# Optimization experiments

Hardware: AMD Instinct MI355X
Metric: run time of the kernel (lower is better)

Reference implementation:

```python
import jax, jax.numpy as jnp
import numpy as np

B, Q, K, D = 8, 2048, 2048, 512

def setup_inputs() -> dict:
    key = jax.random.key(0)
    k1, k2, k3, k4, k5 = jax.random.split(key, 5)
    return {
        "query": jax.random.normal(k1, (B, Q, D), dtype=jnp.float32),
        "key": jax.random.normal(k2, (B, K, D), dtype=jnp.float32),
        "value": jax.random.normal(k3, (B, K, D), dtype=jnp.float32),
        "key_mask": jax.random.randint(k4, (B, K), 0, 2, dtype=jnp.int32),
        "W": jax.random.normal(k5, (D, D), dtype=jnp.float32) / np.sqrt(D),
    }

def reference(query, key, value, key_mask, W):
    # bilinear score: s[b,q,k] = query[b,q,:] @ W @ key[b,k,:]
    scale = 1.0 / jnp.sqrt(jnp.asarray(query.shape[-1], query.dtype))
    qW = jnp.einsum('bqd,de->bqe', query, W)          # [B,Q,D]
    scores = jnp.einsum('bqe,bke->bqk', qW, key)      # [B,Q,K]
    scores = jnp.where(key_mask[:, None, :] == 0, jnp.asarray(-1e20, scores.dtype), scores) * scale
    dist = jax.nn.softmax(scores, axis=-1)            # [B,Q,K]
    context = jnp.einsum('bqk,bkd->bqd', dist, value) # [B,Q,D]
    return context, dist
```

## Files before the change

### kernel.cpp

```cpp
#include <hip/hip_runtime.h>
#include <stdint.h>

#define BB 8
#define QQ 2048
#define KK 2048
#define DD 512

typedef _Float16 f16x8 __attribute__((ext_vector_type(8)));
typedef float f32x4 __attribute__((ext_vector_type(4)));

__device__ __forceinline__ unsigned short f2h(float f) {
    union { _Float16 h; unsigned short u; } x;
    x.h = (_Float16)f;
    return x.u;
}
__device__ __forceinline__ float h2f(unsigned short u) {
    union { unsigned short u; _Float16 h; } x;
    x.u = u;
    return (float)x.h;
}

__device__ __forceinline__ void async16(const unsigned short* g, unsigned short* l) {
    __builtin_amdgcn_global_load_lds(
        (const __attribute__((address_space(1))) unsigned int*)g,
        (__attribute__((address_space(3))) unsigned int*)l, 16, 0, 0);
}

__global__ __launch_bounds__(256) void cvt_f32_f16(const float* __restrict__ in,
                                                   unsigned short* __restrict__ out) {
    size_t i = ((size_t)blockIdx.x * 256 + threadIdx.x) * 8;
    float4 a = *(const float4*)(in + i);
    float4 b = *(const float4*)(in + i + 4);
    uint4 u;
    u.x = (unsigned)f2h(a.x) | ((unsigned)f2h(a.y) << 16);
    u.y = (unsigned)f2h(a.z) | ((unsigned)f2h(a.w) << 16);
    u.z = (unsigned)f2h(b.x) | ((unsigned)f2h(b.y) << 16);
    u.w = (unsigned)f2h(b.z) | ((unsigned)f2h(b.w) << 16);
    *(uint4*)(out + i) = u;
}

__global__ __launch_bounds__(256) void transpose_cvt(const float* __restrict__ in,
                                                     unsigned short* __restrict__ out,
                                                     int R, int C, long inB, long outB) {
    __shared__ float t[32][33];
    const float* ip = in + (size_t)blockIdx.z * inB;
    unsigned short* op = out + (size_t)blockIdx.z * outB;
    int x = threadIdx.x & 31, y0 = threadIdx.x >> 5;
    int c0 = blockIdx.x * 32, r0 = blockIdx.y * 32;
#pragma unroll
    for (int i = 0; i < 32; i += 8)
        t[y0 + i][x] = ip[(size_t)(r0 + y0 + i) * C + c0 + x];
    __syncthreads();
#pragma unroll
    for (int i = 0; i < 32; i += 8)
        op[(size_t)(c0 + y0 + i) * R + r0 + x] = f2h(t[x][y0 + i]);
}

template <int OUTM>
__global__ __launch_bounds__(256) void gemm_bt(const unsigned short* __restrict__ Aall,
                                               const unsigned short* __restrict__ Ball,
                                               void* __restrict__ Call,
                                               const int* __restrict__ maskAll,
                                               float* __restrict__ sums,
                                               int Kred, int lda, int ldb, int ldc,
                                               long aStride, long bStride, long cStride,
                                               int maskStride, float scale) {
    const int gx = gridDim.x, gy = gridDim.y;
    const int nwg = gx * gy * (int)gridDim.z;
    const int p = ((int)blockIdx.z * gy + (int)blockIdx.y) * gx + (int)blockIdx.x;
    const int qch = nwg >> 3, rch = nwg & 7;
    const int xcd = p & 7, ooff = p >> 3;
    const int w = (xcd < rch ? xcd * (qch + 1) : rch * (qch + 1) + (xcd - rch) * qch) + ooff;
    const int b = w / (gx * gy);
    const int rem = w - b * (gx * gy);
    const int my = rem / gx;
    const int nx = rem - my * gx;
    const int m0 = my * 128;
    const int n0 = nx * 128;

    __shared__ unsigned short As[128 * 32];
    __shared__ unsigned short Bs[128 * 32];

    const int tid = threadIdx.x;
    const int lane = tid & 63, wave = tid >> 6;
    const int wm = wave >> 1, wn = wave & 1;
    const int lrow = lane & 15, quad = lane >> 4;

    const int ar = tid >> 2, ac = (tid & 3) * 8;

    const unsigned short* Ab = Aall + (size_t)b * aStride + (size_t)m0 * lda;
    const unsigned short* Bb = Ball + (size_t)b * bStride + (size_t)n0 * ldb;
    unsigned short* AsW = As + wave * 512;
    unsigned short* BsW = Bs + wave * 512;

    f32x4 acc[4][4];
#pragma unroll
    for (int mi = 0; mi < 4; mi++)
#pragma unroll
        for (int ni = 0; ni < 4; ni++)
            acc[mi][ni] = (f32x4){0.f, 0.f, 0.f, 0.f};

    for (int kk = 0; kk < Kred; kk += 32) {
#pragma unroll
        for (int j = 0; j < 2; j++)
            async16(Ab + (size_t)(j * 64 + ar) * lda + kk + ac, AsW + j * 2048);
#pragma unroll
        for (int j = 0; j < 2; j++)
            async16(Bb + (size_t)(j * 64 + ar) * ldb + kk + ac, BsW + j * 2048);
        __syncthreads();

        f16x8 af[4], bfr[4];
#pragma unroll
        for (int i = 0; i < 4; i++)
            af[i] = *(const f16x8*)&As[(wm * 64 + i * 16 + lrow) * 32 + quad * 8];
#pragma unroll
        for (int i = 0; i < 4; i++)
            bfr[i] = *(const f16x8*)&Bs[(wn * 64 + i * 16 + lrow) * 32 + quad * 8];

#pragma unroll
        for (int mi = 0; mi < 4; mi++)
#pragma unroll
            for (int ni = 0; ni < 4; ni++)
                acc[mi][ni] = __builtin_amdgcn_mfma_f32_16x16x32_f16(af[mi], bfr[ni],
                                                                     acc[mi][ni], 0, 0, 0);
        __syncthreads();
    }

#pragma unroll
    for (int mi = 0; mi < 4; mi++) {
        const int gm = m0 + wm * 64 + mi * 16 + quad * 4;
        if constexpr (OUTM == 0) {
            unsigned short* C = (unsigned short*)Call + (size_t)b * cStride;
#pragma unroll
            for (int ni = 0; ni < 4; ni++) {
                int gn = n0 + wn * 64 + ni * 16 + lrow;
#pragma unroll
                for (int r = 0; r < 4; r++)
                    C[(size_t)(gm + r) * ldc + gn] = f2h(acc[mi][ni][r]);
            }
        } else if constexpr (OUTM == 1) {
            unsigned short* C = (unsigned short*)Call + (size_t)b * cStride;
            const int* mk = maskAll + (size_t)b * maskStride;
            float ps[4] = {0.f, 0.f, 0.f, 0.f};
#pragma unroll
            for (int ni = 0; ni < 4; ni++) {
                int gn = n0 + wn * 64 + ni * 16 + lrow;
                bool keep = mk[gn] != 0;
#pragma unroll
                for (int r = 0; r < 4; r++) {
                    float e = keep ? __expf(acc[mi][ni][r] * scale) : 0.f;
                    C[(size_t)(gm + r) * ldc + gn] = f2h(e);
                    ps[r] += e;
                }
            }
#pragma unroll
            for (int off = 1; off < 16; off <<= 1)
#pragma unroll
                for (int r = 0; r < 4; r++) ps[r] += __shfl_xor(ps[r], off);
            if (lrow == 0) {
                float* s = sums + (size_t)b * QQ;
#pragma unroll
                for (int r = 0; r < 4; r++) atomicAdd(&s[gm + r], ps[r]);
            }
        } else {
            float* C = (float*)Call + (size_t)b * cStride;
            const float* s = sums + (size_t)b * QQ;
            float iv[4];
#pragma unroll
            for (int r = 0; r < 4; r++) iv[r] = 1.0f / s[gm + r];
#pragma unroll
            for (int ni = 0; ni < 4; ni++) {
                int gn = n0 + wn * 64 + ni * 16 + lrow;
#pragma unroll
                for (int r = 0; r < 4; r++)
                    C[(size_t)(gm + r) * ldc + gn] = acc[mi][ni][r] * iv[r];
            }
        }
    }
}

__global__ __launch_bounds__(256) void normalize_rows(const unsigned short* __restrict__ expS,
                                                      const float* __restrict__ sums,
                                                      float* __restrict__ dist) {
    const unsigned short* sp = expS + (size_t)blockIdx.x * 2048;
    float* dp = dist + (size_t)blockIdx.x * 2048;
    const float inv = 1.0f / sums[blockIdx.x];
    int tid = threadIdx.x;

    uint4 u = *(const uint4*)(sp + tid * 8);
    float4 o0, o1;
    o0.x = h2f((unsigned short)(u.x & 0xffff)) * inv;
    o0.y = h2f((unsigned short)(u.x >> 16)) * inv;
    o0.z = h2f((unsigned short)(u.y & 0xffff)) * inv;
    o0.w = h2f((unsigned short)(u.y >> 16)) * inv;
    o1.x = h2f((unsigned short)(u.z & 0xffff)) * inv;
    o1.y = h2f((unsigned short)(u.z >> 16)) * inv;
    o1.z = h2f((unsigned short)(u.w & 0xffff)) * inv;
    o1.w = h2f((unsigned short)(u.w >> 16)) * inv;
    *(float4*)(dp + tid * 8) = o0;
    *(float4*)(dp + tid * 8 + 4) = o1;
}

extern "C" void kernel_launch(void* const* d_in, const int* in_sizes, int n_in,
                              void* d_out, int out_size, void* d_ws, size_t ws_size,
                              hipStream_t stream) {
    const float* q    = (const float*)d_in[0];
    const float* k    = (const float*)d_in[1];
    const float* v    = (const float*)d_in[2];
    const int*   mask = (const int*)d_in[3];
    const float* W    = (const float*)d_in[4];

    float* ctx  = (float*)d_out;
    float* dist = ctx + (size_t)BB * QQ * DD;

    unsigned short* ws  = (unsigned short*)d_ws;
    unsigned short* Wt  = ws;
    unsigned short* Qh  = Wt + (size_t)DD * DD;
    unsigned short* Kh  = Qh + (size_t)BB * QQ * DD;
    unsigned short* Vt  = Kh + (size_t)BB * KK * DD;
    unsigned short* qWh = Vt + (size_t)BB * DD * KK;
    unsigned short* Sc  = qWh + (size_t)BB * QQ * DD;
    float* sums = (float*)(Sc + (size_t)BB * QQ * KK);

    const float scale = 0.044194173824159216f;

    (void)hipMemsetAsync(sums, 0, (size_t)BB * QQ * sizeof(float), stream);
    transpose_cvt<<<dim3(DD / 32, DD / 32, 1), 256, 0, stream>>>(W, Wt, DD, DD, 0, 0);
    cvt_f32_f16<<<dim3((BB * QQ * DD / 8) / 256), 256, 0, stream>>>(q, Qh);
    cvt_f32_f16<<<dim3((BB * KK * DD / 8) / 256), 256, 0, stream>>>(k, Kh);
    transpose_cvt<<<dim3(DD / 32, KK / 32, BB), 256, 0, stream>>>(
        v, Vt, KK, DD, (long)KK * DD, (long)DD * KK);
    gemm_bt<0><<<dim3(DD / 128, QQ / 128, BB), 256, 0, stream>>>(
        Qh, Wt, qWh, nullptr, nullptr, DD, DD, DD, DD,
        (long)QQ * DD, 0, (long)QQ * DD, 0, 0.f);
    gemm_bt<1><<<dim3(KK / 128, QQ / 128, BB), 256, 0, stream>>>(
        qWh, Kh, Sc, mask, sums, DD, DD, DD, KK,
        (long)QQ * DD, (long)KK * DD, (long)QQ * KK, KK, scale);
    normalize_rows<<<dim3(BB * QQ), 256, 0, stream>>>(Sc, sums, dist);
    gemm_bt<2><<<dim3(DD / 128, QQ / 128, BB), 256, 0, stream>>>(
        Sc, Vt, ctx, nullptr, sums, KK, KK, KK, DD,
        (long)QQ * KK, (long)DD * KK, (long)QQ * DD, 0, 0.f);
}
```

Measured before the change: 422.3 us.

## Replace score GEMM with 256x256-tile, 4-stage pipelined kernel with XCD-aware remap

The QK^T score GEMM with fused exp/mask/row-sum epilogue moves to a new kernel using 256x256 tiles, 512 threads, a 4-deep async LDS ring buffer with explicit vmcnt waits, and an XCD-aware remapping of workgroup IDs. The larger tile raises data reuse per load and the deeper prefetch hides global latency, aimed at the largest GEMM in the pipeline. In exchange it uses 128KB of LDS per block and many accumulator registers, which may limit occupancy, and it leaves fewer workgroups (512) to spread across CUs.

```diff
diff --git a/kernel.cpp b/kernel.cpp
--- a/kernel.cpp
+++ b/kernel.cpp
@@ -138,30 +138,6 @@
                 for (int r = 0; r < 4; r++)
                     C[(size_t)(gm + r) * ldc + gn] = f2h(acc[mi][ni][r]);
             }
-        } else if constexpr (OUTM == 1) {
-            unsigned short* C = (unsigned short*)Call + (size_t)b * cStride;
-            const int* mk = maskAll + (size_t)b * maskStride;
-            float ps[4] = {0.f, 0.f, 0.f, 0.f};
-#pragma unroll
-            for (int ni = 0; ni < 4; ni++) {
-                int gn = n0 + wn * 64 + ni * 16 + lrow;
-                bool keep = mk[gn] != 0;
-#pragma unroll
-                for (int r = 0; r < 4; r++) {
-                    float e = keep ? __expf(acc[mi][ni][r] * scale) : 0.f;
-                    C[(size_t)(gm + r) * ldc + gn] = f2h(e);
-                    ps[r] += e;
-                }
-            }
-#pragma unroll
-            for (int off = 1; off < 16; off <<= 1)
-#pragma unroll
-                for (int r = 0; r < 4; r++) ps[r] += __shfl_xor(ps[r], off);
-            if (lrow == 0) {
-                float* s = sums + (size_t)b * QQ;
-#pragma unroll
-                for (int r = 0; r < 4; r++) atomicAdd(&s[gm + r], ps[r]);
-            }
         } else {
             float* C = (float*)Call + (size_t)b * cStride;
             const float* s = sums + (size_t)b * QQ;
@@ -175,6 +151,139 @@
                 for (int r = 0; r < 4; r++)
                     C[(size_t)(gm + r) * ldc + gn] = acc[mi][ni][r] * iv[r];
             }
+        }
+    }
+}
+
+__global__ __launch_bounds__(512, 2) void gemm256_exp(
+    const unsigned short* __restrict__ Aall, const unsigned short* __restrict__ Ball,
+    unsigned short* __restrict__ Call, const int* __restrict__ maskAll,
+    float* __restrict__ sums, int Kred, int lda, int ldb, int ldc,
+    long aStride, long bStride, long cStride, int maskStride, float scale) {
+    const int gx = gridDim.x, gy = gridDim.y;
+    const int nwg = gx * gy * (int)gridDim.z;
+    const int p = ((int)blockIdx.z * gy + (int)blockIdx.y) * gx + (int)blockIdx.x;
+    const int qch = nwg >> 3, rch = nwg & 7;
+    const int xcd = p & 7, ooff = p >> 3;
+    const int w = (xcd < rch ? xcd * (qch + 1) : rch * (qch + 1) + (xcd - rch) * qch) + ooff;
+    const int b = w / (gx * gy);
+    const int rem = w - b * (gx * gy);
+    const int my = rem / gx;
+    const int nx = rem - my * gx;
+    const int m0 = my * 256;
+    const int n0 = nx * 256;
+
+    __shared__ unsigned short As[4][256 * 32];
+    __shared__ unsigned short Bs[4][256 * 32];
+
+    const int tid = threadIdx.x;
+    const int lane = tid & 63, wv = tid >> 6;
+    const int wm = wv >> 2, wn = wv & 3;
+    const int lrow = lane & 15, quad = lane >> 4;
+
+    const int sr = lane >> 2;
+    const int ssl = (lane & 3) ^ ((sr >> 1) & 3);
+    const unsigned short* Ab = Aall + (size_t)b * aStride + (size_t)m0 * lda;
+    const unsigned short* Bb = Ball + (size_t)b * bStride + (size_t)n0 * ldb;
+
+    const int NT = Kred >> 5;
+
+    auto stageA = [&](int t) {
+#pragma unroll
+        for (int j = 0; j < 2; j++) {
+            const int c = wv * 2 + j;
+            const int r = c * 16 + sr;
+            async16(Ab + (size_t)r * lda + t * 32 + ssl * 8,
+                    &As[t & 3][c * 512]);
+        }
+    };
+    auto stageB = [&](int t) {
+#pragma unroll
+        for (int j = 0; j < 2; j++) {
+            const int c = wv * 2 + j;
+            const int r = c * 16 + sr;
+            async16(Bb + (size_t)r * ldb + t * 32 + ssl * 8,
+                    &Bs[t & 3][c * 512]);
+        }
+    };
+
+    f32x4 acc[8][4];
+#pragma unroll
+    for (int mi = 0; mi < 8; mi++)
+#pragma unroll
+        for (int ni = 0; ni < 4; ni++)
+            acc[mi][ni] = (f32x4){0.f, 0.f, 0.f, 0.f};
+
+    for (int tt = 0; tt < 3 && tt < NT; ++tt) { stageA(tt); stageB(tt); }
+
+    const int rsw = (lrow >> 1) & 3;
+
+    for (int t = 0; t < NT; ++t) {
+        if (t + 2 < NT)      asm volatile("s_waitcnt vmcnt(8)" ::: "memory");
+        else if (t + 1 < NT) asm volatile("s_waitcnt vmcnt(4)" ::: "memory");
+        else                 asm volatile("s_waitcnt vmcnt(0)" ::: "memory");
+        __builtin_amdgcn_s_barrier();
+        __builtin_amdgcn_sched_barrier(0);
+
+        const unsigned short* Asl = As[t & 3];
+        const unsigned short* Bsl = Bs[t & 3];
+        f16x8 af[4], bfr[4];
+
+        if (t + 3 < NT) stageA(t + 3);
+#pragma unroll
+        for (int ni = 0; ni < 4; ni++)
+            bfr[ni] = *(const f16x8*)&Bsl[(wn * 64 + ni * 16 + lrow) * 32 + ((quad ^ rsw) * 8)];
+#pragma unroll
+        for (int mi = 0; mi < 4; mi++)
+            af[mi] = *(const f16x8*)&Asl[(wm * 128 + mi * 16 + lrow) * 32 + ((quad ^ rsw) * 8)];
+        __builtin_amdgcn_s_setprio(1);
+#pragma unroll
+        for (int mi = 0; mi < 4; mi++)
+#pragma unroll
+            for (int ni = 0; ni < 4; ni++)
+                acc[mi][ni] = __builtin_amdgcn_mfma_f32_16x16x32_f16(af[mi], bfr[ni],
+                                                                     acc[mi][ni], 0, 0, 0);
+        __builtin_amdgcn_s_setprio(0);
+
+        if (t + 3 < NT) stageB(t + 3);
+#pragma unroll
+        for (int mi = 0; mi < 4; mi++)
+            af[mi] = *(const f16x8*)&Asl[(wm * 128 + (mi + 4) * 16 + lrow) * 32 + ((quad ^ rsw) * 8)];
+        __builtin_amdgcn_s_setprio(1);
+#pragma unroll
+        for (int mi = 0; mi < 4; mi++)
+#pragma unroll
+            for (int ni = 0; ni < 4; ni++)
+                acc[mi + 4][ni] = __builtin_amdgcn_mfma_f32_16x16x32_f16(af[mi], bfr[ni],
+                                                                         acc[mi + 4][ni], 0, 0, 0);
+        __builtin_amdgcn_s_setprio(0);
+    }
+
+    unsigned short* C = Call + (size_t)b * cStride;
+    const int* mk = maskAll + (size_t)b * maskStride;
+#pragma unroll
+    for (int mi = 0; mi < 8; mi++) {
+        const int gm = m0 + wm * 128 + mi * 16 + quad * 4;
+        float ps[4] = {0.f, 0.f, 0.f, 0.f};
+#pragma unroll
+        for (int ni = 0; ni < 4; ni++) {
+            int gn = n0 + wn * 64 + ni * 16 + lrow;
+            bool keep = mk[gn] != 0;
+#pragma unroll
+            for (int r = 0; r < 4; r++) {
+                float e = keep ? __expf(acc[mi][ni][r] * scale) : 0.f;
+                C[(size_t)(gm + r) * ldc + gn] = f2h(e);
+                ps[r] += e;
+            }
+        }
+#pragma unroll
+        for (int off = 1; off < 16; off <<= 1)
+#pragma unroll
+            for (int r = 0; r < 4; r++) ps[r] += __shfl_xor(ps[r], off);
+        if (lrow == 0) {
+            float* s = sums + (size_t)b * QQ;
+#pragma unroll
+            for (int r = 0; r < 4; r++) atomicAdd(&s[gm + r], ps[r]);
         }
     }
 }
@@ -233,7 +342,7 @@
     gemm_bt<0><<<dim3(DD / 128, QQ / 128, BB), 256, 0, stream>>>(
         Qh, Wt, qWh, nullptr, nullptr, DD, DD, DD, DD,
         (long)QQ * DD, 0, (long)QQ * DD, 0, 0.f);
-    gemm_bt<1><<<dim3(KK / 128, QQ / 128, BB), 256, 0, stream>>>(
+    gemm256_exp<<<dim3(KK / 256, QQ / 256, BB), 512, 0, stream>>>(
         qWh, Kh, Sc, mask, sums, DD, DD, DD, KK,
         (long)QQ * DD, (long)KK * DD, (long)QQ * KK, KK, scale);
     normalize_rows<<<dim3(BB * QQ), 256, 0, stream>>>(Sc, sums, dist);
```

Measured after the change: 414.1 us. Within noise of the previous version (-1.9%).
